# Performance work log

Measured on AMD Instinct MI355X. Metric: run time of the kernel, lower is better.

The kernel has to match this reference:

```python
import jax, jax.numpy as jnp
import numpy as np

MAX_RADIUS = 5.0
NUM_BASIS = 10
H = 100
# layer configs: (m0_in, m1_in, m0_out, n_gates, m1_out)
LAYERS = [(1, 0, 16, 8, 8), (16, 8, 16, 8, 8), (16, 8, 32, 0, 0)]


def _wtotal(cfg):
    m0i, m1i, m0o, g, m1o = cfg
    m0t = m0o + g
    return m0t * m0i + m0t * m1i + m1o * m0i + 2 * m1o * m1i


def setup_inputs() -> dict:
    key = jax.random.key(0)
    ks = jax.random.split(key, 16)
    N, K = 10000, 16
    inp = {
        "radii": jax.random.normal(ks[0], (N, K, 3), jnp.float32) * 1.5,
        "bs_slice": jax.random.randint(ks[1], (N, K), 0, N),
        "charges": jax.random.randint(ks[2], (N,), 0, 94),
    }
    ki = 3
    for li, cfg in enumerate(LAYERS, 1):
        out_dim = _wtotal(cfg)
        inp[f"l{li}_w1"] = jax.random.normal(ks[ki], (NUM_BASIS, H), jnp.float32) * 0.3; ki += 1
        inp[f"l{li}_b1"] = jnp.zeros((H,), jnp.float32)
        inp[f"l{li}_w2"] = jax.random.normal(ks[ki], (H, H), jnp.float32) * 0.1; ki += 1
        inp[f"l{li}_b2"] = jnp.zeros((H,), jnp.float32)
        inp[f"l{li}_w3"] = jax.random.normal(ks[ki], (H, out_dim), jnp.float32) * 0.1; ki += 1
    return inp


def _radial(r, w1, b1, w2, b2, w3):
    # CosineBasisModel: smooth compact cosine bumps -> 2-hidden-layer relu MLP
    centers = jnp.linspace(0.0, MAX_RADIUS, NUM_BASIS)
    step = MAX_RADIUS / (NUM_BASIS - 1)
    d = (r[:, None] - centers) / step                       # [E, NB]
    basis = jnp.cos(0.5 * jnp.pi * d) ** 2 * (jnp.abs(d) < 1.0)
    h = jax.nn.relu(basis @ w1 + b1)
    h = jax.nn.relu(h @ w2 + b2)
    return h @ w3                                           # [E, total_weights]


def _gated_conv(f0, f1, nbr, rel, cfg, w):
    # gather neighbors -> radial-basis kernel -> equivariant tensor product -> scatter mean -> gated nonlinearity
    m0i, m1i, m0o, g, m1o = cfg
    m0t = m0o + g
    N, K, _ = rel.shape
    E = N * K
    relf = rel.reshape(E, 3)
    r = jnp.linalg.norm(relf, axis=-1)
    u = relf / (r[:, None] + 1e-8)                          # unit vectors ~ Y1
    W = _radial(r, *w)                                      # [E, total]
    idx = nbr.reshape(E)
    g0 = f0[idx]                                            # [E, m0i]
    sizes = [m0t * m0i, m0t * m1i, m1o * m0i, m1o * m1i, m1o * m1i]
    offs = np.cumsum([0] + sizes)
    W00 = W[:, offs[0]:offs[1]].reshape(E, m0t, m0i)
    s = jnp.einsum('eoi,ei->eo', W00, g0)                   # 0->0 path
    if m1i > 0:
        g1 = f1[idx]                                        # [E, m1i, 3]
        W01 = W[:, offs[1]:offs[2]].reshape(E, m0t, m1i)
        s = s + jnp.einsum('eoi,ei->eo', W01, jnp.einsum('eic,ec->ei', g1, u))  # 1->0
    v = None
    if m1o > 0:
        W10 = W[:, offs[2]:offs[3]].reshape(E, m1o, m0i)
        v = jnp.einsum('eoi,ei->eo', W10, g0)[:, :, None] * u[:, None, :]       # 0->1
        if m1i > 0:
            W11a = W[:, offs[3]:offs[4]].reshape(E, m1o, m1i)
            W11b = W[:, offs[4]:offs[5]].reshape(E, m1o, m1i)
            v = v + jnp.einsum('eoi,eic->eoc', W11a, g1)                        # 1->1, l_f=0
            v = v + jnp.einsum('eoi,eic->eoc', W11b, jnp.cross(g1, u[:, None, :]))  # 1->1, l_f=1
    s = s.reshape(N, K, m0t).mean(axis=1)                   # scatter-mean over neighbors
    scalars = jax.nn.relu(s[:, :m0o])
    if m1o > 0:
        gates = jax.nn.sigmoid(s[:, m0o:])
        v = v.reshape(N, K, m1o, 3).mean(axis=1) * gates[:, :, None]
    return scalars, v


def reference(radii, bs_slice, charges,
              l1_w1, l1_b1, l1_w2, l1_b2, l1_w3,
              l2_w1, l2_b1, l2_w2, l2_b2, l2_w3,
              l3_w1, l3_b1, l3_w2, l3_b2, l3_w3):
    params = [(l1_w1, l1_b1, l1_w2, l1_b2, l1_w3),
              (l2_w1, l2_b1, l2_w2, l2_b2, l2_w3),
              (l3_w1, l3_b1, l3_w2, l3_b2, l3_w3)]
    f0 = (charges.astype(jnp.float32) / 94.0 - 0.5)[:, None]  # [N, 1]
    f1 = None
    for cfg, w in zip(LAYERS, params):
        f0 = f0 / 2.0
        if f1 is not None:
            f1 = f1 / 2.0
        f0, f1 = _gated_conv(f0, f1, bs_slice, radii, cfg, w)
    return jnp.mean(f0, axis=0)                              # [32]
```

## Files before the change

kernel.cpp:

```cpp
#include <hip/hip_runtime.h>
#include <math.h>
#include <stdint.h>


#define NTOT  10000
#define EDGES 160000
#define HD    100
#define NBAS  10

typedef __attribute__((ext_vector_type(8))) short short8;
typedef __attribute__((ext_vector_type(4))) float float4v;

__device__ inline unsigned short f2bf(float x) {
  unsigned u = __builtin_bit_cast(unsigned, x);
  u += 0x7fffu + ((u >> 16) & 1u);
  return (unsigned short)(u >> 16);
}
__device__ inline float bf2f(unsigned short b) {
  unsigned u = ((unsigned)b) << 16;
  return __builtin_bit_cast(float, u);
}

__device__ __forceinline__ void dma16(const void* g, void* l) {
  auto gp = (const __attribute__((address_space(1))) unsigned int*)(uintptr_t)g;
  auto lp = (__attribute__((address_space(3))) unsigned int*)(unsigned int)(uintptr_t)l;
  __builtin_amdgcn_global_load_lds(gp, lp, 16, 0, 0);
}
#define WAIT_VM0()  __builtin_amdgcn_s_waitcnt(0x0F70)
#define WAIT_LGKM() __builtin_amdgcn_s_waitcnt(0xC07F)

__device__ inline short8 fragld(const unsigned short* lds, int rbase, int S, int kb, int lane) {
  int r = rbase + (lane & 15);
  int p = kb ^ (r & 15);
  return *(const short8*)(lds + (r * S + p) * 8);
}

__device__ inline unsigned short bt_elem(const float* __restrict__ w, int Ks, int Ns,
                                         int off01, int off10, int g) {
  int slot = g >> 3, j = g & 7;
  int grp = slot >> 10, rem = slot & 1023;
  int row = rem >> 4, x = rem & 15;
  int kb = x ^ (row & 15);
  int k = kb * 8 + j;
  int cg = grp * 64 + row, n = cg;
  if (cg >= off01 && cg < off10) {
    int cl = cg & 63;
    int wv = cl >> 4, qd = (cl >> 2) & 3, r = cl & 3;
    int t = (cg - off01) >> 6;
    n = off01 + (8 * t + wv + 4 * (qd >> 1)) * 8 + (qd & 1) * 4 + r;
  }
  float v = (k < Ks && n < Ns) ? w[k * Ns + n] : 0.f;
  return f2bf(v);
}

__device__ inline unsigned short w1_elem(const float* __restrict__ w1,
                                         const float* __restrict__ b1, int g) {
  int s = g >> 3, j = g & 7;
  int row = s >> 2, x = s & 3;
  int q = x ^ (row & 3);
  int k = q * 8 + j;
  int n = row;
  float v = 0.f; int lo = 0;
  if (k < 10)       { v = (n < HD) ? w1[k * HD + n] : 0.f; lo = 0; }
  else if (k < 20)  { v = (n < HD) ? w1[(k - 10) * HD + n] : 0.f; lo = 0; }
  else if (k < 30)  { v = (n < HD) ? w1[(k - 20) * HD + n] : 0.f; lo = 1; }
  else if (k == 30) { v = (n < HD) ? b1[n] : 0.f; lo = 0; }
  else              { v = (n < HD) ? b1[n] : 0.f; lo = 1; }
  unsigned short hi = f2bf(v);
  return lo ? f2bf(v - bf2f(hi)) : hi;
}

__global__ void prep_all(const float* __restrict__ w2a, const float* __restrict__ w2b,
                         const float* __restrict__ w2c,
                         const float* __restrict__ w3a, const float* __restrict__ w3b,
                         const float* __restrict__ w3c,
                         const float* __restrict__ w1a, const float* __restrict__ w1b,
                         const float* __restrict__ w1c,
                         const float* __restrict__ b1a, const float* __restrict__ b1b,
                         const float* __restrict__ b1c,
                         unsigned short* __restrict__ bt2, unsigned short* __restrict__ bt31,
                         unsigned short* __restrict__ bt32, unsigned short* __restrict__ bt33,
                         unsigned short* __restrict__ w1i1, unsigned short* __restrict__ w1i2,
                         unsigned short* __restrict__ w1i3) {
  int g = blockIdx.x * 256 + threadIdx.x;
  if (g < 16384) { bt2[g]         = bt_elem(w2a, 100, 100, 0, 0, g); return; }  g -= 16384;
  if (g < 16384) { bt2[16384 + g] = bt_elem(w2b, 100, 100, 0, 0, g); return; }  g -= 16384;
  if (g < 16384) { bt2[32768 + g] = bt_elem(w2c, 100, 100, 0, 0, g); return; }  g -= 16384;
  if (g < 8192)  { bt31[g] = bt_elem(w3a, 100, 32,  0,   0,   g); return; }     g -= 8192;
  if (g < 106496){ bt32[g] = bt_elem(w3b, 100, 832, 384, 576, g); return; }     g -= 106496;
  if (g < 98304) { bt33[g] = bt_elem(w3c, 100, 768, 512, 768, g); return; }     g -= 98304;
  if (g < 4096)  { w1i1[g] = w1_elem(w1a, b1a, g); return; }                    g -= 4096;
  if (g < 4096)  { w1i2[g] = w1_elem(w1b, b1b, g); return; }                    g -= 4096;
  if (g < 4096)  { w1i3[g] = w1_elem(w1c, b1c, g); }
}

template<int M0I, int M1I, int M0O, int NG, int M1O>
__global__ __launch_bounds__(256, 4) void layer_fused(
    const float* __restrict__ radii, const int* __restrict__ nbr,
    const int* __restrict__ charges,
    const float* __restrict__ f0prev, const float* __restrict__ f1prev,
    const unsigned short* __restrict__ w1i,
    const unsigned short* __restrict__ bt2, const float* __restrict__ b2,
    const unsigned short* __restrict__ bt3,
    float* __restrict__ f0next, float* __restrict__ f1next)
{
  constexpr int M0T = M0O + NG;
  constexpr int O   = M0T * M0I + M0T * M1I + M1O * M0I + 2 * M1O * M1I;
  constexpr int OFF01  = M0T * M0I;
  constexpr int OFF10  = OFF01 + M0T * M1I;
  constexpr int OFF11A = OFF10 + M1O * M0I;
  constexpr int OFF11B = OFF11A + M1O * M1I;
  constexpr int NCH  = (O + 63) / 64;
  constexpr int SSTR = M0T + 1;
  constexpr int ASTR = 9;
  constexpr int VSTR = 25;

  __shared__ __align__(16) unsigned short bufB[64 * 128];
  __shared__ __align__(16) unsigned short bufA[64 * 128];
  __shared__ float sh_s[64 * SSTR];
  __shared__ float sh_a10[(M1O > 0) ? 64 * ASTR : 1];
  __shared__ float sh_u[64 * 3];
  __shared__ int   sh_idx[64];
  __shared__ float b2s[128];

  float* sh_g0f = (float*)(bufA + 6144);
  float* sh_vf  = (float*)(bufA + 4096);

  const int tid  = threadIdx.x;
  const int lane = tid & 63, w = tid >> 6;
  const int quad = lane >> 4, ln15 = lane & 15;
  const int eg0  = blockIdx.x * 64;

  {
    const char* gw1 = (const char*)w1i + (size_t)w * 2048 + lane * 16;
    char* lw1 = (char*)bufA + w * 2048;
    dma16(gw1, lw1);
    dma16(gw1 + 1024, lw1 + 1024);
    const char* gw2 = (const char*)bt2 + (size_t)w * 4096 + lane * 16;
    char* lw2 = (char*)bufB + w * 4096;
    #pragma unroll
    for (int i = 0; i < 4; ++i) dma16(gw2 + i * 1024, lw2 + i * 1024);
  }

  if (tid < 64) {
    float x = radii[(size_t)(eg0 + tid) * 3 + 0];
    float y = radii[(size_t)(eg0 + tid) * 3 + 1];
    float z = radii[(size_t)(eg0 + tid) * 3 + 2];
    float rr = sqrtf(x * x + y * y + z * z);
    float inv = 1.0f / (rr + 1e-8f);
    sh_u[tid * 3 + 0] = x * inv;
    sh_u[tid * 3 + 1] = y * inv;
    sh_u[tid * 3 + 2] = z * inv;
    sh_idx[tid] = nbr[eg0 + tid];
    float bas[NBAS];
    constexpr float STEP = 5.0f / 9.0f;
    #pragma unroll
    for (int nb = 0; nb < NBAS; ++nb) {
      float d = (rr - (float)nb * STEP) / STEP;
      float c = cosf(1.5707964f * d);
      bas[nb] = (fabsf(d) < 1.0f) ? c * c : 0.0f;
    }
    unsigned short bh[NBAS], bl[NBAS];
    #pragma unroll
    for (int nb = 0; nb < NBAS; ++nb) {
      bh[nb] = f2bf(bas[nb]);
      bl[nb] = f2bf(bas[nb] - bf2f(bh[nb]));
    }
    const unsigned short ONE = 0x3F80;
    short8 q0 = {(short)bh[0], (short)bh[1], (short)bh[2], (short)bh[3],
                 (short)bh[4], (short)bh[5], (short)bh[6], (short)bh[7]};
    short8 q1 = {(short)bh[8], (short)bh[9], (short)bl[0], (short)bl[1],
                 (short)bl[2], (short)bl[3], (short)bl[4], (short)bl[5]};
    short8 q2 = {(short)bl[6], (short)bl[7], (short)bl[8], (short)bl[9],
                 (short)bh[0], (short)bh[1], (short)bh[2], (short)bh[3]};
    short8 q3 = {(short)bh[4], (short)bh[5], (short)bh[6], (short)bh[7],
                 (short)bh[8], (short)bh[9], (short)ONE, (short)ONE};
    unsigned short* bt = bufA + 4096;
    *(short8*)&bt[(tid * 4 + (0 ^ (tid & 3))) * 8] = q0;
    *(short8*)&bt[(tid * 4 + (1 ^ (tid & 3))) * 8] = q1;
    *(short8*)&bt[(tid * 4 + (2 ^ (tid & 3))) * 8] = q2;
    *(short8*)&bt[(tid * 4 + (3 ^ (tid & 3))) * 8] = q3;
  }
  if (tid < 128) b2s[tid] = (tid < HD) ? b2[tid] : 0.f;
  WAIT_VM0();
  __syncthreads();

  float4v acc1[2][4];
  {
    short8 basf[4];
    const unsigned short* basT = bufA + 4096;
    #pragma unroll
    for (int eg = 0; eg < 4; ++eg) {
      int e = eg * 16 + ln15;
      basf[eg] = *(const short8*)&basT[(e * 4 + (quad ^ (e & 3))) * 8];
    }
    #pragma unroll
    for (int h = 0; h < 2; ++h) {
      int m = h * 64 + w * 16 + ln15;
      short8 af = *(const short8*)&bufA[(m * 4 + (quad ^ (m & 3))) * 8];
      #pragma unroll
      for (int eg = 0; eg < 4; ++eg) {
        float4v z4 = {0.f, 0.f, 0.f, 0.f};
        acc1[h][eg] = __builtin_amdgcn_mfma_f32_16x16x32_bf16(af, basf[eg], z4, 0, 0, 0);
      }
    }
  }
  if constexpr (M0I > 1) {
    #pragma unroll
    for (int it = 0; it < 4; ++it) {
      int p = tid + 256 * it;
      int e = p >> 4, i = p & 15;
      sh_g0f[p] = 0.5f * f0prev[sh_idx[e] * M0I + i];
    }
  } else {
    if (tid < 64) sh_g0f[tid] = 0.5f * ((float)charges[sh_idx[tid]] / 94.0f - 0.5f);
  }
  __syncthreads();

  float g0r[4][(M0I > 1) ? 4 : 1];
  #pragma unroll
  for (int eg = 0; eg < 4; ++eg) {
    int e = eg * 16 + ln15;
    if constexpr (M0I > 1) {
      #pragma unroll
      for (int r = 0; r < 4; ++r) g0r[eg][r] = sh_g0f[e * 16 + quad * 4 + r];
    } else {
      g0r[eg][0] = sh_g0f[e];
    }
  }
  __syncthreads();

  #pragma unroll
  for (int h = 0; h < 2; ++h)
    #pragma unroll
    for (int eg = 0; eg < 4; ++eg) {
      int e = eg * 16 + ln15;
      #pragma unroll
      for (int p = 0; p < 2; ++p) {
        int col = h * 64 + w * 16 + quad * 4 + 2 * p;
        unsigned lo = f2bf(fmaxf(acc1[h][eg][2 * p],     0.f));
        unsigned hi = f2bf(fmaxf(acc1[h][eg][2 * p + 1], 0.f));
        int kb = col >> 3, j = col & 7;
        *(unsigned*)&bufA[(e * 16 + (kb ^ (e & 15))) * 8 + j] = lo | (hi << 16);
      }
    }
  __syncthreads();

  short8 h1f[4][4];
  #pragma unroll
  for (int eg = 0; eg < 4; ++eg)
    #pragma unroll
    for (int kk = 0; kk < 4; ++kk)
      h1f[eg][kk] = fragld(bufA, eg * 16, 16, kk * 4 + quad, lane);
  __syncthreads();

  #pragma unroll
  for (int t = 0; t < 2; ++t) {
    WAIT_VM0();
    short8 bf[4];
    #pragma unroll
    for (int ks = 0; ks < 4; ++ks) bf[ks] = fragld(bufB, w * 16, 16, ks * 4 + quad, lane);
    WAIT_LGKM();
    {
      const char* src = (t == 0) ? ((const char*)bt2 + 16384) : (const char*)bt3;
      const char* g = src + (size_t)w * 4096 + lane * 16;
      char* l = (char*)bufB + w * 4096;
      #pragma unroll
      for (int i = 0; i < 4; ++i) dma16(g + i * 1024, l + i * 1024);
    }
    float4v acc[4];
    #pragma unroll
    for (int eg = 0; eg < 4; ++eg) acc[eg] = (float4v){0.f, 0.f, 0.f, 0.f};
    #pragma unroll
    for (int ks = 0; ks < 4; ++ks)
      #pragma unroll
      for (int eg = 0; eg < 4; ++eg)
        acc[eg] = __builtin_amdgcn_mfma_f32_16x16x32_bf16(bf[ks], h1f[eg][ks], acc[eg], 0, 0, 0);
    {
      int colb = t * 64 + w * 16 + quad * 4;
      float b0 = b2s[colb], b1v = b2s[colb + 1], b2v = b2s[colb + 2], b3 = b2s[colb + 3];
      #pragma unroll
      for (int eg = 0; eg < 4; ++eg) {
        int e = eg * 16 + ln15;
        unsigned l0 = f2bf(fmaxf(acc[eg][0] + b0, 0.f));
        unsigned h0 = f2bf(fmaxf(acc[eg][1] + b1v, 0.f));
        unsigned l1 = f2bf(fmaxf(acc[eg][2] + b2v, 0.f));
        unsigned h1_ = f2bf(fmaxf(acc[eg][3] + b3, 0.f));
        int kb = colb >> 3, j = colb & 7;
        *(unsigned*)&bufA[(e * 16 + (kb ^ (e & 15))) * 8 + j]   = l0 | (h0 << 16);
        int colc = colb + 2, kb2 = colc >> 3, j2 = colc & 7;
        *(unsigned*)&bufA[(e * 16 + (kb2 ^ (e & 15))) * 8 + j2] = l1 | (h1_ << 16);
      }
    }
  }
  __syncthreads();

  short8 h2f[4][4];
  #pragma unroll
  for (int eg = 0; eg < 4; ++eg)
    #pragma unroll
    for (int kk = 0; kk < 4; ++kk)
      h2f[eg][kk] = fragld(bufA, eg * 16, 16, kk * 4 + quad, lane);

  float tax[(M1I > 0) ? 4 : 1][(M1I > 0) ? 4 : 1];
  float tay[(M1I > 0) ? 4 : 1][(M1I > 0) ? 4 : 1];
  float taz[(M1I > 0) ? 4 : 1][(M1I > 0) ? 4 : 1];
  float ux[4], uy[4], uz[4];
  float p1r[(M1I > 0) ? 4 : 1][(M1I > 0) ? 4 : 1];
  if constexpr (M1I > 0) {
    __syncthreads();
    float4v* tbl = (float4v*)bufA;
    #pragma unroll
    for (int it = 0; it < 2; ++it) {
      int p = tid + 256 * it;
      int e = p >> 3, i = p & 7;
      const float* g = f1prev + (size_t)(sh_idx[e] * M1I + i) * 3;
      tbl[e * 8 + (i ^ (e & 7))] = (float4v){0.5f * g[0], 0.5f * g[1], 0.5f * g[2], 0.f};
    }
    __syncthreads();
    #pragma unroll
    for (int eg = 0; eg < 4; ++eg) {
      int e = eg * 16 + ln15;
      ux[eg] = sh_u[e * 3 + 0]; uy[eg] = sh_u[e * 3 + 1]; uz[eg] = sh_u[e * 3 + 2];
      #pragma unroll
      for (int r = 0; r < 4; ++r) {
        int i = (quad & 1) * 4 + r;
        float4v tv = tbl[e * 8 + (i ^ (e & 7))];
        tax[eg][r] = tv[0]; tay[eg][r] = tv[1]; taz[eg][r] = tv[2];
        p1r[eg][r] = tv[0] * ux[eg] + tv[1] * uy[eg] + tv[2] * uz[eg];
      }
    }
    __syncthreads();
  }

  for (int c = 0; c < NCH; ++c) {
    const int c0 = c * 64;
    WAIT_VM0();
    short8 bf[4];
    #pragma unroll
    for (int ks = 0; ks < 4; ++ks) bf[ks] = fragld(bufB, w * 16, 16, ks * 4 + quad, lane);
    WAIT_LGKM();
    if (c + 1 < NCH) {
      const char* g = (const char*)bt3 + (size_t)(c + 1) * 16384 + (size_t)w * 4096 + lane * 16;
      char* l = (char*)bufB + w * 4096;
      #pragma unroll
      for (int i = 0; i < 4; ++i) dma16(g + i * 1024, l + i * 1024);
    }
    float4v acc[4];
    #pragma unroll
    for (int eg = 0; eg < 4; ++eg) acc[eg] = (float4v){0.f, 0.f, 0.f, 0.f};
    #pragma unroll
    for (int ks = 0; ks < 4; ++ks)
      #pragma unroll
      for (int eg = 0; eg < 4; ++eg)
        acc[eg] = __builtin_amdgcn_mfma_f32_16x16x32_bf16(bf[ks], h2f[eg][ks], acc[eg], 0, 0, 0);

    if constexpr (M0I == 1) {
      if (w < 2) {
        #pragma unroll
        for (int eg = 0; eg < 4; ++eg) {
          int e = eg * 16 + ln15;
          #pragma unroll
          for (int r = 0; r < 4; ++r) {
            int col = w * 16 + quad * 4 + r;
            float val = acc[eg][r] * g0r[eg][0];
            if (col < OFF01) sh_s[e * SSTR + col] = val;
            else             sh_a10[e * ASTR + (col - OFF01)] = val;
          }
        }
      }
    } else {
      if (c0 < OFF01) {
        const int o = (c0 >> 4) + w;
        float part[4];
        #pragma unroll
        for (int eg = 0; eg < 4; ++eg)
          part[eg] = fmaf(acc[eg][0], g0r[eg][0], fmaf(acc[eg][1], g0r[eg][1],
                     fmaf(acc[eg][2], g0r[eg][2], acc[eg][3] * g0r[eg][3])));
        #pragma unroll
        for (int eg = 0; eg < 4; ++eg) {
          part[eg] += __shfl_xor(part[eg], 16);
          part[eg] += __shfl_xor(part[eg], 32);
        }
        if (quad == 0) {
          #pragma unroll
          for (int eg = 0; eg < 4; ++eg)
            sh_s[(eg * 16 + ln15) * SSTR + o] = part[eg];
        }
      } else if (c0 < OFF10) {
        const int t = (c0 - OFF01) >> 6;
        const int o = 8 * t + w + 4 * (quad >> 1);
        float part[4];
        #pragma unroll
        for (int eg = 0; eg < 4; ++eg)
          part[eg] = fmaf(acc[eg][0], p1r[eg][0], fmaf(acc[eg][1], p1r[eg][1],
                     fmaf(acc[eg][2], p1r[eg][2], acc[eg][3] * p1r[eg][3])));
        #pragma unroll
        for (int eg = 0; eg < 4; ++eg) part[eg] += __shfl_xor(part[eg], 16);
        if ((quad & 1) == 0) {
          #pragma unroll
          for (int eg = 0; eg < 4; ++eg)
            sh_s[(eg * 16 + ln15) * SSTR + o] += part[eg];
        }
      } else if constexpr (M1O > 0) {
        if (c0 < OFF11A) {
          const int o = ((c0 - OFF10) >> 4) + w;
          float part[4];
          #pragma unroll
          for (int eg = 0; eg < 4; ++eg)
            part[eg] = fmaf(acc[eg][0], g0r[eg][0], fmaf(acc[eg][1], g0r[eg][1],
                       fmaf(acc[eg][2], g0r[eg][2], acc[eg][3] * g0r[eg][3])));
          #pragma unroll
          for (int eg = 0; eg < 4; ++eg) {
            part[eg] += __shfl_xor(part[eg], 16);
            part[eg] += __shfl_xor(part[eg], 32);
          }
          if (quad == 0) {
            #pragma unroll
            for (int eg = 0; eg < 4; ++eg)
              sh_a10[(eg * 16 + ln15) * ASTR + o] = part[eg];
          }
        } else {
          const bool is_b = (c0 >= OFF11B);
          const int o = ((c0 - (is_b ? OFF11B : OFF11A)) >> 3) + 2 * w + (quad >> 1);
          #pragma unroll
          for (int eg = 0; eg < 4; ++eg) {
            int e = eg * 16 + ln15;
            float px = 0.f, py = 0.f, pz = 0.f;
            #pragma unroll
            for (int r = 0; r < 4; ++r) {
              float cx, cy, cz;
              if (is_b) {
                cx = tay[eg][r] * uz[eg] - taz[eg][r] * uy[eg];
                cy = taz[eg][r] * ux[eg] - tax[eg][r] * uz[eg];
                cz = tax[eg][r] * uy[eg] - tay[eg][r] * ux[eg];
              } else {
                cx = tax[eg][r]; cy = tay[eg][r]; cz = taz[eg][r];
              }
              px = fmaf(acc[eg][r], cx, px);
              py = fmaf(acc[eg][r], cy, py);
              pz = fmaf(acc[eg][r], cz, pz);
            }
            px += __shfl_xor(px, 16);
            py += __shfl_xor(py, 16);
            pz += __shfl_xor(pz, 16);
            if ((quad & 1) == 0) {
              float* vp = &sh_vf[e * VSTR + o * 3];
              if (is_b) { vp[0] += px; vp[1] += py; vp[2] += pz; }
              else      { vp[0] = px;  vp[1] = py;  vp[2] = pz; }
            }
          }
        }
      }
    }
  }
  __syncthreads();

  if (tid < 4 * M0T) {
    const int nl = tid / M0T;
    const int o  = tid - nl * M0T;
    float ssum = 0.0f;
    for (int k = 0; k < 16; ++k) ssum += sh_s[(nl * 16 + k) * SSTR + o];
    const float sm = ssum * 0.0625f;
    const int n = blockIdx.x * 4 + nl;
    if (o < M0O) {
      f0next[n * M0O + o] = fmaxf(sm, 0.0f);
    } else if constexpr (M1O > 0) {
      const int og = o - M0O;
      const float gate = 1.0f / (1.0f + expf(-sm));
      float vx = 0.f, vy = 0.f, vz = 0.f;
      for (int k = 0; k < 16; ++k) {
        int e = nl * 16 + k;
        float a = sh_a10[e * ASTR + og];
        float bx = 0.f, by = 0.f, bz = 0.f;
        if constexpr (M1I > 0) {
          bx = sh_vf[e * VSTR + og * 3 + 0];
          by = sh_vf[e * VSTR + og * 3 + 1];
          bz = sh_vf[e * VSTR + og * 3 + 2];
        }
        vx += fmaf(a, sh_u[e * 3 + 0], bx);
        vy += fmaf(a, sh_u[e * 3 + 1], by);
        vz += fmaf(a, sh_u[e * 3 + 2], bz);
      }
      const float sc = gate * 0.0625f;
      f1next[(n * M1O + og) * 3 + 0] = vx * sc;
      f1next[(n * M1O + og) * 3 + 1] = vy * sc;
      f1next[(n * M1O + og) * 3 + 2] = vz * sc;
    }
  }
}

__global__ void reduce_kernel(const float* __restrict__ f0c, float* __restrict__ out) {
  __shared__ float red[256];
  const int o = blockIdx.x;
  float s = 0.0f;
  for (int n = threadIdx.x; n < NTOT; n += 256) s += f0c[n * 32 + o];
  red[threadIdx.x] = s;
  __syncthreads();
  for (int w = 128; w > 0; w >>= 1) {
    if (threadIdx.x < w) red[threadIdx.x] += red[threadIdx.x + w];
    __syncthreads();
  }
  if (threadIdx.x == 0) out[o] = red[0] / (float)NTOT;
}

extern "C" void kernel_launch(void* const* d_in, const int* in_sizes, int n_in,
                              void* d_out, int out_size, void* d_ws, size_t ws_size,
                              hipStream_t stream) {
  const float* radii   = (const float*)d_in[0];
  const int*   nbr     = (const int*)d_in[1];
  const int*   charges = (const int*)d_in[2];
  const float* w1l[3] = {(const float*)d_in[3],  (const float*)d_in[8],  (const float*)d_in[13]};
  const float* b1l[3] = {(const float*)d_in[4],  (const float*)d_in[9],  (const float*)d_in[14]};
  const float* w2l[3] = {(const float*)d_in[5],  (const float*)d_in[10], (const float*)d_in[15]};
  const float* b2l[3] = {(const float*)d_in[6],  (const float*)d_in[11], (const float*)d_in[16]};
  const float* w3l[3] = {(const float*)d_in[7],  (const float*)d_in[12], (const float*)d_in[17]};

  char* ws = (char*)d_ws;
  size_t off = 0;
  float* f0a = (float*)(ws + off); off += (size_t)NTOT * 16 * 4;
  float* f1a = (float*)(ws + off); off += (size_t)NTOT * 24 * 4;
  float* f0b = (float*)(ws + off); off += (size_t)NTOT * 16 * 4;
  float* f1b = (float*)(ws + off); off += (size_t)NTOT * 24 * 4;
  float* f0c = (float*)(ws + off); off += (size_t)NTOT * 32 * 4;
  unsigned short* bt2  = (unsigned short*)(ws + off); off += (size_t)3 * 16384 * 2;
  unsigned short* bt31 = (unsigned short*)(ws + off); off += (size_t)8192 * 2;
  unsigned short* bt32 = (unsigned short*)(ws + off); off += (size_t)106496 * 2;
  unsigned short* bt33 = (unsigned short*)(ws + off); off += (size_t)98304 * 2;
  unsigned short* w1i1 = (unsigned short*)(ws + off); off += (size_t)4096 * 2;
  unsigned short* w1i2 = (unsigned short*)(ws + off); off += (size_t)4096 * 2;
  unsigned short* w1i3 = (unsigned short*)(ws + off); off += (size_t)4096 * 2;

  prep_all<<<1072, 256, 0, stream>>>(w2l[0], w2l[1], w2l[2], w3l[0], w3l[1], w3l[2],
                                     w1l[0], w1l[1], w1l[2], b1l[0], b1l[1], b1l[2],
                                     bt2, bt31, bt32, bt33, w1i1, w1i2, w1i3);

  constexpr int NBLK = EDGES / 64;

  layer_fused<1, 0, 16, 8, 8><<<NBLK, 256, 0, stream>>>(
      radii, nbr, charges, nullptr, nullptr,
      w1i1, bt2, b2l[0], bt31, f0a, f1a);

  layer_fused<16, 8, 16, 8, 8><<<NBLK, 256, 0, stream>>>(
      radii, nbr, charges, f0a, f1a,
      w1i2, bt2 + 16384, b2l[1], bt32, f0b, f1b);

  layer_fused<16, 8, 32, 0, 0><<<NBLK, 256, 0, stream>>>(
      radii, nbr, charges, f0b, f1b,
      w1i3, bt2 + 32768, b2l[2], bt33, f0c, nullptr);

  reduce_kernel<<<32, 256, 0, stream>>>(f0c, (float*)d_out);
}
```

Before: 275.7 us.

## Load MLP weight fragments directly from global memory instead of LDS staging

The bf16 weight matrices for the second and third radial MLP layers are pre-packed in fragment order (lane, k-step, wave, chunk), so each lane reads its MFMA B operand as contiguous short8 loads straight from global memory. The LDS buffer bufB, the async global-to-LDS DMA prefetch, and the associated waitcnt barriers are removed. This frees LDS, which may raise occupancy, and drops the LDS round-trip. The cost is that global load latency is no longer hidden behind the previous chunk's compute and now relies on L2/cache hits.

```diff
diff --git a/kernel.cpp b/kernel.cpp
--- a/kernel.cpp
+++ b/kernel.cpp
@@ -26,8 +26,7 @@
   auto lp = (__attribute__((address_space(3))) unsigned int*)(unsigned int)(uintptr_t)l;
   __builtin_amdgcn_global_load_lds(gp, lp, 16, 0, 0);
 }
-#define WAIT_VM0()  __builtin_amdgcn_s_waitcnt(0x0F70)
-#define WAIT_LGKM() __builtin_amdgcn_s_waitcnt(0xC07F)
+#define WAIT_VM0() __builtin_amdgcn_s_waitcnt(0x0F70)
 
 __device__ inline short8 fragld(const unsigned short* lds, int rbase, int S, int kb, int lane) {
   int r = rbase + (lane & 15);
@@ -37,17 +36,16 @@
 
 __device__ inline unsigned short bt_elem(const float* __restrict__ w, int Ks, int Ns,
                                          int off01, int off10, int g) {
-  int slot = g >> 3, j = g & 7;
-  int grp = slot >> 10, rem = slot & 1023;
-  int row = rem >> 4, x = rem & 15;
-  int kb = x ^ (row & 15);
-  int k = kb * 8 + j;
-  int cg = grp * 64 + row, n = cg;
+  int j = g & 7, slot = g >> 3;
+  int lane = slot & 63, ks = (slot >> 6) & 3, wv = (slot >> 8) & 3, c = slot >> 10;
+  int quad = lane >> 4, ln = lane & 15;
+  int k = (ks * 4 + quad) * 8 + j;
+  int cg = c * 64 + wv * 16 + ln, n = cg;
   if (cg >= off01 && cg < off10) {
     int cl = cg & 63;
-    int wv = cl >> 4, qd = (cl >> 2) & 3, r = cl & 3;
+    int w_ = cl >> 4, qd = (cl >> 2) & 3, r = cl & 3;
     int t = (cg - off01) >> 6;
-    n = off01 + (8 * t + wv + 4 * (qd >> 1)) * 8 + (qd & 1) * 4 + r;
+    n = off01 + (8 * t + w_ + 4 * (qd >> 1)) * 8 + (qd & 1) * 4 + r;
   }
   float v = (k < Ks && n < Ns) ? w[k * Ns + n] : 0.f;
   return f2bf(v);
@@ -115,7 +113,6 @@
   constexpr int ASTR = 9;
   constexpr int VSTR = 25;
 
-  __shared__ __align__(16) unsigned short bufB[64 * 128];
   __shared__ __align__(16) unsigned short bufA[64 * 128];
   __shared__ float sh_s[64 * SSTR];
   __shared__ float sh_a10[(M1O > 0) ? 64 * ASTR : 1];
@@ -136,10 +133,6 @@
     char* lw1 = (char*)bufA + w * 2048;
     dma16(gw1, lw1);
     dma16(gw1 + 1024, lw1 + 1024);
-    const char* gw2 = (const char*)bt2 + (size_t)w * 4096 + lane * 16;
-    char* lw2 = (char*)bufB + w * 4096;
-    #pragma unroll
-    for (int i = 0; i < 4; ++i) dma16(gw2 + i * 1024, lw2 + i * 1024);
   }
 
   if (tid < 64) {
@@ -256,17 +249,11 @@
 
   #pragma unroll
   for (int t = 0; t < 2; ++t) {
-    WAIT_VM0();
     short8 bf[4];
-    #pragma unroll
-    for (int ks = 0; ks < 4; ++ks) bf[ks] = fragld(bufB, w * 16, 16, ks * 4 + quad, lane);
-    WAIT_LGKM();
     {
-      const char* src = (t == 0) ? ((const char*)bt2 + 16384) : (const char*)bt3;
-      const char* g = src + (size_t)w * 4096 + lane * 16;
-      char* l = (char*)bufB + w * 4096;
-      #pragma unroll
-      for (int i = 0; i < 4; ++i) dma16(g + i * 1024, l + i * 1024);
+      const short8* wp = (const short8*)bt2 + (size_t)(t * 4 + w) * 256 + lane;
+      #pragma unroll
+      for (int ks = 0; ks < 4; ++ks) bf[ks] = wp[ks * 64];
     }
     float4v acc[4];
     #pragma unroll
@@ -335,16 +322,11 @@
 
   for (int c = 0; c < NCH; ++c) {
     const int c0 = c * 64;
-    WAIT_VM0();
     short8 bf[4];
-    #pragma unroll
-    for (int ks = 0; ks < 4; ++ks) bf[ks] = fragld(bufB, w * 16, 16, ks * 4 + quad, lane);
-    WAIT_LGKM();
-    if (c + 1 < NCH) {
-      const char* g = (const char*)bt3 + (size_t)(c + 1) * 16384 + (size_t)w * 4096 + lane * 16;
-      char* l = (char*)bufB + w * 4096;
-      #pragma unroll
-      for (int i = 0; i < 4; ++i) dma16(g + i * 1024, l + i * 1024);
+    {
+      const short8* wp = (const short8*)bt3 + (size_t)(c * 4 + w) * 256 + lane;
+      #pragma unroll
+      for (int ks = 0; ks < 4; ++ks) bf[ks] = wp[ks * 64];
     }
     float4v acc[4];
     #pragma unroll
```

After: 424.0 us. +53.8%, slower.
